# Optimization experiments

Hardware: AMD Instinct MI355X
Metric: run time of the kernel (lower is better)

Reference implementation:

```python
import jax, jax.numpy as jnp
import numpy as np

H = 128          # hidden_channels
L = 2            # num_layers
E = 400000       # edges per relation
N_ATOM = 600000
N = (20000, 20000, 10000)  # node counts: 0=Chemical, 1=Gene, 2=Assay
OUT = 2          # out_channels
# (src_type, dst_type) per relation, matching the HeteroConv_att dict order
RELS = ((0,2),(0,2),(0,1),(0,1),(0,1),(2,1),(1,1),(2,0),(2,0),(1,0),(1,0),(1,0),(1,2))
R = len(RELS)
NEG_SLOPE = 0.2  # GATv2 LeakyReLU slope


def setup_inputs() -> dict:
    key = jax.random.key(0)
    ks = jax.random.split(key, 16)
    sc = 1.0 / np.sqrt(H)
    x_atom  = jax.random.normal(ks[0], (N_ATOM, H), jnp.float32)
    x_chem  = jax.random.normal(ks[1], (N[0], H), jnp.float32)
    x_gene  = jax.random.normal(ks[2], (N[1], H), jnp.float32)
    x_assay = jax.random.normal(ks[3], (N[2], H), jnp.float32)
    hyper_dst = jax.random.randint(ks[4], (N_ATOM,), 0, N[0], jnp.int32)
    ei = []
    for r, (s, d) in enumerate(RELS):
        src = jax.random.randint(jax.random.fold_in(ks[5], 2 * r), (E,), 0, N[s], jnp.int32)
        dst = jax.random.randint(jax.random.fold_in(ks[5], 2 * r + 1), (E,), 0, N[d], jnp.int32)
        ei.append(jnp.stack([src, dst]))
    edge_index_rel = jnp.stack(ei)  # [R, 2, E]
    W_mol = jax.random.normal(ks[6], (H, H), jnp.float32) * sc
    Wl    = jax.random.normal(ks[7], (L, R, H, H), jnp.float32) * sc
    Wr    = jax.random.normal(ks[8], (L, R, H, H), jnp.float32) * sc
    bl    = jnp.zeros((L, R, H), jnp.float32)
    br    = jnp.zeros((L, R, H), jnp.float32)
    att_a = jax.random.normal(ks[9], (L, R, H), jnp.float32) * sc
    cb    = jnp.zeros((L, R, H), jnp.float32)  # GATv2 output bias
    ln_g  = jnp.ones((L, 3, H), jnp.float32)   # LayerNorm gamma per (layer, node type)
    ln_b  = jnp.zeros((L, 3, H), jnp.float32)
    Wp    = jax.random.normal(ks[10], (H, OUT), jnp.float32) * sc
    bp    = jnp.zeros((OUT,), jnp.float32)
    return dict(x_atom=x_atom, x_chem=x_chem, x_gene=x_gene, x_assay=x_assay,
                W_mol=W_mol, Wl=Wl, Wr=Wr, bl=bl, br=br, att_a=att_a, cb=cb,
                ln_g=ln_g, ln_b=ln_b, Wp=Wp, bp=bp,
                hyper_dst=hyper_dst, edge_index_rel=edge_index_rel,
                chemical_label_task=0)


def _gatv2(x_src, x_dst, src, dst, Wl, Wr, bl, br, a, cb, n_dst):
    # GATv2Conv, single head, add_self_loops=False, share_weights=False
    xl = x_src @ Wl + bl                              # [Ns, H]
    xr = x_dst @ Wr + br                              # [Nd, H]
    e = jax.nn.leaky_relu(xl[src] + xr[dst], NEG_SLOPE) @ a  # [E]
    m = jax.ops.segment_max(e, dst, num_segments=n_dst)      # per-dst max
    ex = jnp.exp(e - m[dst])
    denom = jax.ops.segment_sum(ex, dst, num_segments=n_dst)
    alpha = ex / jnp.maximum(denom[dst], 1e-16)
    out = jax.ops.segment_sum(alpha[:, None] * xl[src], dst, num_segments=n_dst)
    return out + cb


def _layernorm(x, g, b):
    mu = x.mean(-1, keepdims=True)
    v = ((x - mu) ** 2).mean(-1, keepdims=True)
    return (x - mu) / jnp.sqrt(v + 1e-5) * g + b


def reference(x_atom, x_chem, x_gene, x_assay, W_mol, Wl, Wr, bl, br, att_a, cb,
              ln_g, ln_b, Wp, bp, hyper_dst, edge_index_rel, chemical_label_task):
    # molecular encoder (modeled as a linear projection over atom features)
    atom_enc = x_atom @ W_mol
    # bottom_up: mean-aggregate Atom -> Chemical, then add dst (Chemical) features
    ones = jnp.ones((N_ATOM,), atom_enc.dtype)
    cnt = jax.ops.segment_sum(ones, hyper_dst, num_segments=N[0])
    mean_agg = jax.ops.segment_sum(atom_enc, hyper_dst, num_segments=N[0]) \
               / jnp.maximum(cnt, 1.0)[:, None]
    xs = [mean_agg + x_chem, x_gene, x_assay]  # Chemical, Gene, Assay
    for l in range(L):
        agg = [jnp.zeros((N[t], H), x_chem.dtype) for t in range(3)]
        for r, (s, d) in enumerate(RELS):
            src = edge_index_rel[r, 0]
            dst = edge_index_rel[r, 1]
            out = _gatv2(xs[s], xs[d], src, dst, Wl[l, r], Wr[l, r], bl[l, r],
                         br[l, r], att_a[l, r], cb[l, r], N[d])
            agg[d] = agg[d] + out  # aggr='sum' across relations per dst type
        xs = [jax.nn.relu(_layernorm(agg[t], ln_g[l, t], ln_b[l, t])) for t in range(3)]
    return xs[0] @ Wp + bp  # pred_layer on Chemical nodes -> [N_chem, OUT]
```

## Files before the change

kernel.cpp:

```cpp
#include <hip/hip_runtime.h>
#include <math.h>

#define H 128
#define NLAYER 2
#define EDG 400000
#define NATOM 600000
#define NREL 13
#define SEGS 14
#define RDX 256
#define TILE 4096
#define NPAIR 5800000

typedef unsigned short u16;
typedef unsigned int u32;
using short8  = __attribute__((ext_vector_type(8))) short;
using ushort8 = __attribute__((ext_vector_type(8))) unsigned short;
using floatx4 = __attribute__((ext_vector_type(4))) float;

static constexpr int NODE_N[3]   = {20000, 20000, 10000};
static constexpr int TYPE_OFF[3] = {0, 20000, 40000};
static constexpr int SRC_T[NREL] = {0,0,0,0,0,2,1,2,2,1,1,1,1};
static constexpr int DST_T[NREL] = {2,2,1,1,1,1,1,0,0,0,0,0,2};

static constexpr int NREL_OF[3]    = {5, 5, 3};
static constexpr int RELS_OF[3][5] = {{7,8,9,10,11},{2,3,4,5,6},{0,1,12}};

static constexpr int XOFF_S[NREL] = {0,20000,40000,60000,80000,100000,110000,130000,140000,150000,170000,190000,210000};
static constexpr int XOFF_D[NREL] = {0,10000,20000,40000,60000,80000,100000,120000,140000,160000,180000,200000,220000};
#define XTOT 230000

static constexpr int SEG_N[SEGS]  = {20000,10000,10000,20000,20000,20000,20000,20000,20000,20000,20000,20000,20000,10000};
static constexpr int SEG_RO[SEGS] = {0,20001,30002,40003,60004,80005,100006,120007,140008,160009,180010,200011,220012,240013};
#define RP_TOTAL 250016

static constexpr int    SLEN[SEGS] = {600000,EDG,EDG,EDG,EDG,EDG,EDG,EDG,EDG,EDG,EDG,EDG,EDG,EDG};
static constexpr size_t SPOFF[SEGS] = {0,600000,1000000,1400000,1800000,2200000,2600000,3000000,3400000,3800000,4200000,4600000,5000000,5400000};
static constexpr int    RNB[SEGS]  = {147,98,98,98,98,98,98,98,98,98,98,98,98,98};
static constexpr int    RBHOFF[SEGS] = {0,37632,62720,87808,112896,137984,163072,188160,213248,238336,263424,288512,313600,338688};
#define BH_TOTAL 363776

__device__ __forceinline__ float wave_reduce_sum(float v) {
#pragma unroll
  for (int off = 32; off > 0; off >>= 1) v += __shfl_xor(v, off, 64);
  return v;
}

__device__ __forceinline__ u16 f2bf(float f) {
  union { float f; u32 u; } c; c.f = f;
  u32 u = c.u + 0x7fffu + ((c.u >> 16) & 1u);
  return (u16)(u >> 16);
}
__device__ __forceinline__ float bf2f(u16 h) { union { u32 i; float f; } c; c.i = (u32)h << 16; return c.f; }
__device__ __forceinline__ float bflo(u32 u) { union { u32 i; float f; } c; c.i = u << 16; return c.f; }
__device__ __forceinline__ float bfhi(u32 u) { union { u32 i; float f; } c; c.i = u & 0xffff0000u; return c.f; }


__global__ __launch_bounds__(256) void radix_init(const int* __restrict__ hyper,
                                                  const int* __restrict__ ei,
                                                  int2* __restrict__ A) {
  int s = blockIdx.y;
  int i = blockIdx.x * 256 + threadIdx.x;
  if (i >= SLEN[s]) return;
  int2 p;
  if (s == 0) { p.x = hyper[i]; p.y = i; }
  else {
    int r = s - 1;
    p.x = ei[(size_t)(r * 2 + 1) * EDG + i];
    p.y = ei[(size_t)(r * 2) * EDG + i];
  }
  A[SPOFF[s] + i] = p;
}

__global__ __launch_bounds__(256) void radix_count(const int2* __restrict__ in,
                                                   int* __restrict__ bh, int shift) {
  int s = blockIdx.y, bx = blockIdx.x;
  int nb = RNB[s];
  if (bx >= nb) return;
  __shared__ int h[RDX];
  int t = threadIdx.x;
  h[t] = 0;
  __syncthreads();
  int len = SLEN[s];
  size_t poff = SPOFF[s];
#pragma unroll
  for (int i = 0; i < 16; ++i) {
    int p = bx * TILE + i * 256 + t;
    if (p < len) atomicAdd(&h[(in[poff + p].x >> shift) & 255], 1);
  }
  __syncthreads();
  bh[RBHOFF[s] + t * nb + bx] = h[t];
}

__global__ __launch_bounds__(256) void radix_scan(int* __restrict__ bh) {
  int s = blockIdx.x;
  int total = RNB[s] * RDX;
  int off = RBHOFF[s];
  __shared__ int sums[256];
  int t = threadIdx.x;
  int chunk = (total + 255) >> 8;
  int b = t * chunk, e = min(b + chunk, total);
  int acc = 0;
  for (int i = b; i < e; ++i) acc += bh[off + i];
  sums[t] = acc;
  __syncthreads();
  for (int o2 = 1; o2 < 256; o2 <<= 1) {
    int v = (t >= o2) ? sums[t - o2] : 0;
    __syncthreads();
    sums[t] += v;
    __syncthreads();
  }
  int pre = t ? sums[t - 1] : 0;
  for (int i = b; i < e; ++i) { int c = bh[off + i]; bh[off + i] = pre; pre += c; }
}

__global__ __launch_bounds__(256) void radix_scatter(const int2* __restrict__ in,
                                                     int2* __restrict__ out,
                                                     const int* __restrict__ bh, int shift) {
  int s = blockIdx.y, bx = blockIdx.x;
  int nb = RNB[s];
  if (bx >= nb) return;
  __shared__ int2 stg[TILE];
  __shared__ int wc[4][RDX];
  __shared__ int pw[4][RDX];
  __shared__ int basev[RDX];
  __shared__ int lstart[RDX];
  __shared__ int delta[RDX];
  int t = threadIdx.x;
  int lane = t & 63, w = t >> 6;
  unsigned long long lmask = (1ull << lane) - 1ull;
  int len = SLEN[s];
  size_t poff = SPOFF[s];
  int2 kv[16]; int dg[16]; int rk[16];
  basev[t] = 0;
#pragma unroll
  for (int i = 0; i < 16; ++i) {
    int p = bx * TILE + i * 256 + t;
    kv[i] = (p < len) ? in[poff + p] : make_int2(0, 0);
  }
  __syncthreads();
  for (int i = 0; i < 16; ++i) {
    int p = bx * TILE + i * 256 + t;
    bool valid = p < len;
    int d = (kv[i].x >> shift) & 255;
    wc[0][t] = 0; wc[1][t] = 0; wc[2][t] = 0; wc[3][t] = 0;
    __syncthreads();
    unsigned long long m = __ballot(valid);
#pragma unroll
    for (int b2 = 0; b2 < 8; ++b2) {
      unsigned long long bal = __ballot((d >> b2) & 1);
      m &= ((d >> b2) & 1) ? bal : ~bal;
    }
    int riw = __popcll(m & lmask);
    if (valid && riw == 0) wc[w][d] = __popcll(m);
    __syncthreads();
    int s0 = 0;
#pragma unroll
    for (int ww = 0; ww < 4; ++ww) { pw[ww][t] = s0; s0 += wc[ww][t]; }
    __syncthreads();
    dg[i] = d;
    rk[i] = basev[d] + pw[w][d] + riw;
    __syncthreads();
    basev[t] += s0;
    __syncthreads();
  }
  int tot = basev[t];
  pw[0][t] = tot;
  __syncthreads();
  for (int o2 = 1; o2 < 256; o2 <<= 1) {
    int v = (t >= o2) ? pw[0][t - o2] : 0;
    __syncthreads();
    pw[0][t] += v;
    __syncthreads();
  }
  int ls = pw[0][t] - tot;
  lstart[t] = ls;
  delta[t] = bh[RBHOFF[s] + t * nb + bx] - ls;
  __syncthreads();
#pragma unroll
  for (int i = 0; i < 16; ++i) {
    int p = bx * TILE + i * 256 + t;
    if (p < len) stg[lstart[dg[i]] + rk[i]] = kv[i];
  }
  __syncthreads();
  int vc = min(len - bx * TILE, TILE);
#pragma unroll
  for (int i = 0; i < 16; ++i) {
    int p = i * 256 + t;
    if (p < vc) {
      int2 pr = stg[p];
      int d = (pr.x >> shift) & 255;
      out[poff + delta[d] + p] = pr;
    }
  }
}

__global__ __launch_bounds__(256) void build_rp(const int2* __restrict__ A, int* __restrict__ rp) {
  int s = blockIdx.y;
  int len = SLEN[s];
  int j = blockIdx.x * 256 + threadIdx.x;
  if (j >= len) return;
  size_t poff = SPOFF[s];
  int ro = SEG_RO[s];
  int k = A[poff + j].x;
  int kprev = (j == 0) ? -1 : A[poff + j - 1].x;
  for (int d = kprev + 1; d <= k; ++d) rp[ro + d] = j;
  if (j == len - 1) {
    int n = SEG_N[s];
    for (int d = k + 1; d <= n; ++d) rp[ro + d] = len;
  }
}


__global__ __launch_bounds__(256) void mean_atoms(const float* __restrict__ x_atom,
                                                  const int* __restrict__ rp,
                                                  const int2* __restrict__ pairs,
                                                  float* __restrict__ Mean) {
  int wave = (blockIdx.x * blockDim.x + threadIdx.x) >> 6;
  int lane = threadIdx.x & 63;
  int g = lane >> 5, l32 = lane & 31;
  int chem = wave * 2 + g;
  if (chem >= 20000) return;
  int b = rp[chem], e = rp[chem + 1];
  float4 s = make_float4(0.f, 0.f, 0.f, 0.f);
  for (int j = b; j < e; ++j) {
    int a = pairs[j].y;
    float4 v = *(const float4*)(x_atom + (size_t)a * H + l32 * 4);
    s.x += v.x; s.y += v.y; s.z += v.z; s.w += v.w;
  }
  float inv = 1.0f / fmaxf((float)(e - b), 1.0f);
  float4 o; o.x = s.x * inv; o.y = s.y * inv; o.z = s.z * inv; o.w = s.w * inv;
  *(float4*)(Mean + (size_t)chem * H + l32 * 4) = o;
}


__global__ __launch_bounds__(256) void proj_kernel(
    const float* __restrict__ X, const float* __restrict__ W,
    const float* __restrict__ Res, float* __restrict__ Y, int N) {
  int r0 = blockIdx.x * 64;
  if (r0 >= N) return;
  __shared__ float Xs[64][132];
  int tid = threadIdx.x;
#pragma unroll
  for (int i = 0; i < 8; ++i) {
    int f = tid + 256 * i;
    int row = f >> 5, c4 = (f & 31) << 2;
    float4 v = make_float4(0.f, 0.f, 0.f, 0.f);
    if (r0 + row < N) v = *(const float4*)(X + (size_t)(r0 + row) * H + c4);
    *(float4*)&Xs[row][c4] = v;
  }
  __syncthreads();
  int trow = tid >> 5, tcol = tid & 31;
  float acc[8][4] = {};
#pragma unroll 4
  for (int k = 0; k < 128; ++k) {
    float4 w = *(const float4*)(W + k * H + tcol * 4);
#pragma unroll
    for (int i = 0; i < 8; ++i) {
      float xv = Xs[trow * 8 + i][k];
      acc[i][0] = fmaf(xv, w.x, acc[i][0]);
      acc[i][1] = fmaf(xv, w.y, acc[i][1]);
      acc[i][2] = fmaf(xv, w.z, acc[i][2]);
      acc[i][3] = fmaf(xv, w.w, acc[i][3]);
    }
  }
#pragma unroll
  for (int i = 0; i < 8; ++i) {
    int row = r0 + trow * 8 + i;
    if (row < N) {
      float4 rv = *(const float4*)(Res + (size_t)row * H + tcol * 4);
      float4 ov;
      ov.x = acc[i][0] + rv.x; ov.y = acc[i][1] + rv.y;
      ov.z = acc[i][2] + rv.z; ov.w = acc[i][3] + rv.w;
      *(float4*)(Y + (size_t)row * H + tcol * 4) = ov;
    }
  }
}


__global__ __launch_bounds__(256) void conv_xs(const float* __restrict__ xs,
                                               const float* __restrict__ x_gene,
                                               const float* __restrict__ x_assay,
                                               u16* __restrict__ xsb) {
  int idx = (blockIdx.x * 256 + threadIdx.x) * 4;
  if (idx >= 50000 * H) return;
  int row = idx >> 7;
  const float* src;
  if (row < 20000)      src = xs + idx;
  else if (row < 40000) src = x_gene + (idx - 20000 * H);
  else                  src = x_assay + (idx - 40000 * H);
  float4 v = *(const float4*)src;
  u32 p0 = (u32)f2bf(v.x) | ((u32)f2bf(v.y) << 16);
  u32 p1 = (u32)f2bf(v.z) | ((u32)f2bf(v.w) << 16);
  u32* o = (u32*)(xsb + idx);
  o[0] = p0; o[1] = p1;
}

__global__ __launch_bounds__(256) void conv_weights(const float* __restrict__ Wl,
                                                    const float* __restrict__ Wr,
                                                    u16* __restrict__ WB) {
  int mat = blockIdx.x;
  int side = blockIdx.y;
  const float* W = (side ? Wr : Wl) + (size_t)mat * H * H;
  u16* O = WB + ((size_t)mat * 2 + side) * H * H;
  for (int f = threadIdx.x; f < H * H; f += 256) {
    int n = f >> 7, k = f & 127;
    O[f] = f2bf(W[k * H + n]);
  }
}


__global__ __launch_bounds__(256) void proj_mfma(
    const u16* __restrict__ xsb, const u16* __restrict__ WB,
    const float* __restrict__ bl, const float* __restrict__ br,
    u16* __restrict__ XLb, u16* __restrict__ XRb, int layer) {
  int by = blockIdx.y;
  int r = by >> 1, side = by & 1;
  int typ = side ? DST_T[r] : SRC_T[r];
  int N = NODE_N[typ];
  int r0 = blockIdx.x * 64;
  if (r0 >= N) return;
  const u16* X = xsb + (size_t)TYPE_OFF[typ] * H;
  const u16* W = WB + ((size_t)(layer * NREL + r) * 2 + side) * H * H;
  const float* bias = (side ? br : bl) + (size_t)(layer * NREL + r) * H;
  u16* Y = side ? (XRb + (size_t)XOFF_D[r] * H) : (XLb + (size_t)XOFF_S[r] * H);

  __shared__ u16 Xs[64 * 136];
  __shared__ u16 Ws[128 * 136];
  int tid = threadIdx.x;
#pragma unroll
  for (int i = 0; i < 4; ++i) {
    int f = tid + 256 * i;
    int row = f >> 4, seg = f & 15;
    ushort8 v = {};
    if (r0 + row < N) v = *(const ushort8*)(X + (size_t)(r0 + row) * H + seg * 8);
    *(ushort8*)(Xs + row * 136 + seg * 8) = v;
  }
#pragma unroll
  for (int i = 0; i < 8; ++i) {
    int f = tid + 256 * i;
    int row = f >> 4, seg = f & 15;
    *(ushort8*)(Ws + row * 136 + seg * 8) = *(const ushort8*)(W + row * H + seg * 8);
  }
  __syncthreads();

  int w = tid >> 6, lane = tid & 63;
  int g = lane >> 4, l16 = lane & 15;
  floatx4 acc[4][2] = {};
#pragma unroll
  for (int kt = 0; kt < 4; ++kt) {
    int k0 = kt * 32 + g * 8;
    short8 a[4], b[2];
#pragma unroll
    for (int rt = 0; rt < 4; ++rt) a[rt] = *(const short8*)(Xs + (rt * 16 + l16) * 136 + k0);
#pragma unroll
    for (int ct = 0; ct < 2; ++ct) b[ct] = *(const short8*)(Ws + (w * 32 + ct * 16 + l16) * 136 + k0);
#pragma unroll
    for (int rt = 0; rt < 4; ++rt)
#pragma unroll
      for (int ct = 0; ct < 2; ++ct)
        acc[rt][ct] = __builtin_amdgcn_mfma_f32_16x16x32_bf16(a[rt], b[ct], acc[rt][ct], 0, 0, 0);
  }
  __syncthreads();
  float bv0 = bias[w * 32 + l16];
  float bv1 = bias[w * 32 + 16 + l16];
#pragma unroll
  for (int rt = 0; rt < 4; ++rt)
#pragma unroll
    for (int ct = 0; ct < 2; ++ct) {
      float bv = ct ? bv1 : bv0;
      int col = w * 32 + ct * 16 + l16;
#pragma unroll
      for (int reg = 0; reg < 4; ++reg) {
        int row = rt * 16 + g * 4 + reg;
        Xs[row * 136 + col] = f2bf(acc[rt][ct][reg] + bv);
      }
    }
  __syncthreads();
#pragma unroll
  for (int i = 0; i < 4; ++i) {
    int f = tid + 256 * i;
    int row = f >> 4, seg = f & 15;
    if (r0 + row < N)
      *(ushort8*)(Y + (size_t)(r0 + row) * H + seg * 8) = *(const ushort8*)(Xs + row * 136 + seg * 8);
  }
}


__global__ __launch_bounds__(256) void gat_fused(
    const u16* __restrict__ XLb, const u16* __restrict__ XRb,
    const int* __restrict__ rp, const int2* __restrict__ A,
    const float* __restrict__ att_a, const float* __restrict__ cbv,
    float* __restrict__ agg, int layer, int dt) {
  int wave = (blockIdx.x * blockDim.x + threadIdx.x) >> 6;
  int lane = threadIdx.x & 63;
  int g = lane >> 4, l16 = lane & 15;
  int d = wave * 4 + g;
  int Nd = NODE_N[dt];
  bool dv = d < Nd;
  int dd = dv ? d : Nd - 1;
  float o[8] = {};
  int nr = NREL_OF[dt];
  for (int rr = 0; rr < nr; ++rr) {
    int r = RELS_OF[dt][rr];
    size_t wi = (size_t)layer * NREL + r;
    const u16* XL = XLb + (size_t)XOFF_S[r] * H;
    const u16* XR = XRb + (size_t)XOFF_D[r] * H;
    ushort8 uxr = *(const ushort8*)(XR + (size_t)dd * H + l16 * 8);
    float xr[8];
#pragma unroll
    for (int c = 0; c < 8; ++c) xr[c] = bf2f((u16)uxr[c]);
    float4 a0 = *(const float4*)(att_a + wi * H + l16 * 8);
    float4 a1 = *(const float4*)(att_a + wi * H + l16 * 8 + 4);
    float av[8] = {a0.x, a0.y, a0.z, a0.w, a1.x, a1.y, a1.z, a1.w};
    const int* rpr = rp + SEG_RO[r + 1];
    const int2* pe = A + SPOFF[r + 1];
    int b = dv ? rpr[dd] : 0;
    int e = dv ? rpr[dd + 1] : 0;
    float m = -1e30f, s = 0.f;
    float V[8] = {};
    for (int j = b; j < e; ++j) {
      int src = pe[j].y;
      ushort8 uxl = *(const ushort8*)(XL + (size_t)src * H + l16 * 8);
      float xl[8];
      float t = 0.f;
#pragma unroll
      for (int c = 0; c < 8; ++c) {
        xl[c] = bf2f((u16)uxl[c]);
        float v = xl[c] + xr[c];
        float lr = v > 0.f ? v : 0.2f * v;
        t = fmaf(av[c], lr, t);
      }
      t += __shfl_xor(t, 1, 64);
      t += __shfl_xor(t, 2, 64);
      t += __shfl_xor(t, 4, 64);
      t += __shfl_xor(t, 8, 64);
      float nm = fmaxf(m, t);
      float sc = __expf(m - nm);
      float wgt = __expf(t - nm);
      s = s * sc + wgt;
#pragma unroll
      for (int c = 0; c < 8; ++c) V[c] = V[c] * sc + wgt * xl[c];
      m = nm;
    }
    if (s > 0.f) {
      float inv = 1.0f / s;
#pragma unroll
      for (int c = 0; c < 8; ++c) o[c] += V[c] * inv;
    }
    float4 c0 = *(const float4*)(cbv + wi * H + l16 * 8);
    float4 c1 = *(const float4*)(cbv + wi * H + l16 * 8 + 4);
    o[0] += c0.x; o[1] += c0.y; o[2] += c0.z; o[3] += c0.w;
    o[4] += c1.x; o[5] += c1.y; o[6] += c1.z; o[7] += c1.w;
  }
  if (dv) {
    float* ap = agg + (size_t)(TYPE_OFF[dt] + d) * H + l16 * 8;
    *(float4*)ap       = make_float4(o[0], o[1], o[2], o[3]);
    *(float4*)(ap + 4) = make_float4(o[4], o[5], o[6], o[7]);
  }
}


__global__ __launch_bounds__(256) void ln_relu_kernel(const float* __restrict__ agg,
                                                      const float* __restrict__ g,
                                                      const float* __restrict__ b,
                                                      u16* __restrict__ xsb) {
  int row = (blockIdx.x * blockDim.x + threadIdx.x) >> 6;
  int lane = threadIdx.x & 63;
  if (row >= 50000) return;
  int t = row < 20000 ? 0 : (row < 40000 ? 1 : 2);
  float2 x = *(const float2*)(agg + (size_t)row * H + 2 * lane);
  float mu = wave_reduce_sum(x.x + x.y) * (1.f / 128.f);
  float d0 = x.x - mu, d1 = x.y - mu;
  float var = wave_reduce_sum(d0 * d0 + d1 * d1) * (1.f / 128.f);
  float inv = 1.0f / sqrtf(var + 1e-5f);
  float2 gg = *(const float2*)(g + t * H + 2 * lane);
  float2 bb = *(const float2*)(b + t * H + 2 * lane);
  float o0 = fmaxf(d0 * inv * gg.x + bb.x, 0.f);
  float o1 = fmaxf(d1 * inv * gg.y + bb.y, 0.f);
  u32 pk = (u32)f2bf(o0) | ((u32)f2bf(o1) << 16);
  *(u32*)(xsb + (size_t)row * H + 2 * lane) = pk;
}


__global__ __launch_bounds__(256) void pred_kernel(const u16* __restrict__ xsb,
                                                   const float* __restrict__ Wp,
                                                   const float* __restrict__ bp,
                                                   float* __restrict__ out) {
  int row = (blockIdx.x * blockDim.x + threadIdx.x) >> 6;
  int lane = threadIdx.x & 63;
  if (row >= 20000) return;
  u32 u = *(const u32*)(xsb + (size_t)row * H + 2 * lane);
  float x0 = bflo(u), x1 = bfhi(u);
  float4 w = *(const float4*)(Wp + 4 * lane);
  float pA = x0 * w.x + x1 * w.z;
  float pB = x0 * w.y + x1 * w.w;
  pA = wave_reduce_sum(pA);
  pB = wave_reduce_sum(pB);
  if (lane == 0) {
    out[(size_t)row * 2 + 0] = pA + bp[0];
    out[(size_t)row * 2 + 1] = pB + bp[1];
  }
}


extern "C" void kernel_launch(void* const* d_in, const int* in_sizes, int n_in,
                              void* d_out, int out_size, void* d_ws, size_t ws_size,
                              hipStream_t stream) {
  (void)in_sizes; (void)n_in; (void)out_size; (void)ws_size;
  const float* x_atom  = (const float*)d_in[0];
  const float* x_chem  = (const float*)d_in[1];
  const float* x_gene  = (const float*)d_in[2];
  const float* x_assay = (const float*)d_in[3];
  const float* W_mol   = (const float*)d_in[4];
  const float* Wl      = (const float*)d_in[5];
  const float* Wr      = (const float*)d_in[6];
  const float* bl      = (const float*)d_in[7];
  const float* br      = (const float*)d_in[8];
  const float* att_a   = (const float*)d_in[9];
  const float* cb      = (const float*)d_in[10];
  const float* ln_g    = (const float*)d_in[11];
  const float* ln_b    = (const float*)d_in[12];
  const float* Wp      = (const float*)d_in[13];
  const float* bp      = (const float*)d_in[14];
  const int*   hyper   = (const int*)d_in[15];
  const int*   ei      = (const int*)d_in[16];
  float* out = (float*)d_out;

  float* ws = (float*)d_ws;
  size_t o = 0;
  float* xs   = ws + o; o += (size_t)50000 * H;
  float* agg  = ws + o; o += (size_t)50000 * H;
  float* Mean = ws + o; o += (size_t)20000 * H;
  int2*  A    = (int2*)(ws + o); o += (size_t)2 * NPAIR;
  int2*  Bp2  = (int2*)(ws + o); o += (size_t)2 * NPAIR;
  int*   rp   = (int*)(ws + o); o += RP_TOTAL;
  int*   bh   = (int*)(ws + o); o += BH_TOTAL;
  u16*   xsb  = (u16*)(ws + o); o += (size_t)50000 * H / 2;
  u16*   WB   = (u16*)(ws + o); o += (size_t)52 * H * H / 2;
  u16*   XLb  = (u16*)(ws + o); o += (size_t)XTOT * H / 2;
  u16*   XRb  = (u16*)(ws + o); o += (size_t)XTOT * H / 2;

  dim3 b256(256);

  radix_init<<<dim3(2344, SEGS), b256, 0, stream>>>(hyper, ei, A);
  radix_count<<<dim3(147, SEGS), b256, 0, stream>>>(A, bh, 0);
  radix_scan<<<SEGS, b256, 0, stream>>>(bh);
  radix_scatter<<<dim3(147, SEGS), b256, 0, stream>>>(A, Bp2, bh, 0);
  radix_count<<<dim3(147, SEGS), b256, 0, stream>>>(Bp2, bh, 8);
  radix_scan<<<SEGS, b256, 0, stream>>>(bh);
  radix_scatter<<<dim3(147, SEGS), b256, 0, stream>>>(Bp2, A, bh, 8);
  build_rp<<<dim3(2344, SEGS), b256, 0, stream>>>(A, rp);

  mean_atoms<<<dim3(20000 / 8), b256, 0, stream>>>(x_atom, rp, A, Mean);
  proj_kernel<<<dim3(313), b256, 0, stream>>>(Mean, W_mol, x_chem, xs, 20000);
  conv_xs<<<dim3(6250), b256, 0, stream>>>(xs, x_gene, x_assay, xsb);
  conv_weights<<<dim3(26, 2), b256, 0, stream>>>(Wl, Wr, WB);

  for (int l = 0; l < NLAYER; ++l) {
    proj_mfma<<<dim3(313, 26), b256, 0, stream>>>(xsb, WB, bl, br, XLb, XRb, l);
    for (int dt = 0; dt < 3; ++dt)
      gat_fused<<<dim3((NODE_N[dt] + 15) / 16), b256, 0, stream>>>(
          XLb, XRb, rp, A, att_a, cb, agg, l, dt);
    ln_relu_kernel<<<dim3(50000 / 4), b256, 0, stream>>>(agg, ln_g + l * 3 * H, ln_b + l * 3 * H, xsb);
  }
  pred_kernel<<<dim3(20000 / 4), b256, 0, stream>>>(xsb, Wp, bp, out);
}
```

Baseline: 1.710 ms.

## Pack edge pairs into 32-bit keys, merge GAT launches, unroll edge loop by two

Edge (dst,src) pairs are packed into a single u32 (dst<<15|src) instead of int2, which halves radix-sort and CSR traffic. The sort uses bits 15 and 23 as digit positions so the two passes key on dst. The three per-type GAT launches are merged into one launch over all 50000 nodes. The GAT inner loop processes two edges per iteration so loads overlap and one online-softmax rescale serves both edges. The chemical projection writes bf16 directly, removing the fp32 xs buffer and part of the conversion pass; the packing relies on src<32768 and dst<131072.

```diff
diff --git a/kernel.cpp b/kernel.cpp
--- a/kernel.cpp
+++ b/kernel.cpp
@@ -9,7 +9,6 @@
 #define SEGS 14
 #define RDX 256
 #define TILE 4096
-#define NPAIR 5800000
 
 typedef unsigned short u16;
 typedef unsigned int u32;
@@ -33,9 +32,8 @@
 static constexpr int SEG_RO[SEGS] = {0,20001,30002,40003,60004,80005,100006,120007,140008,160009,180010,200011,220012,240013};
 #define RP_TOTAL 250016
 
-static constexpr int    SLEN[SEGS] = {600000,EDG,EDG,EDG,EDG,EDG,EDG,EDG,EDG,EDG,EDG,EDG,EDG,EDG};
-static constexpr size_t SPOFF[SEGS] = {0,600000,1000000,1400000,1800000,2200000,2600000,3000000,3400000,3800000,4200000,4600000,5000000,5400000};
-static constexpr int    RNB[SEGS]  = {147,98,98,98,98,98,98,98,98,98,98,98,98,98};
+static constexpr int    SLEN[SEGS]   = {600000,EDG,EDG,EDG,EDG,EDG,EDG,EDG,EDG,EDG,EDG,EDG,EDG,EDG};
+static constexpr int    RNB[SEGS]    = {147,98,98,98,98,98,98,98,98,98,98,98,98,98};
 static constexpr int    RBHOFF[SEGS] = {0,37632,62720,87808,112896,137984,163072,188160,213248,238336,263424,288512,313600,338688};
 #define BH_TOTAL 363776
 
@@ -54,38 +52,40 @@
 __device__ __forceinline__ float bflo(u32 u) { union { u32 i; float f; } c; c.i = u << 16; return c.f; }
 __device__ __forceinline__ float bfhi(u32 u) { union { u32 i; float f; } c; c.i = u & 0xffff0000u; return c.f; }
 
-
-__global__ __launch_bounds__(256) void radix_init(const int* __restrict__ hyper,
-                                                  const int* __restrict__ ei,
-                                                  int2* __restrict__ A) {
-  int s = blockIdx.y;
+__device__ __forceinline__ int digof(u32 v, int shift) { return (int)((v >> shift) & 255u); }
+__device__ __forceinline__ int digof(int2 v, int shift) { return (v.x >> shift) & 255; }
+
+
+__global__ __launch_bounds__(256) void radix_init_a(const int* __restrict__ hyper, int2* __restrict__ Aa) {
   int i = blockIdx.x * 256 + threadIdx.x;
-  if (i >= SLEN[s]) return;
-  int2 p;
-  if (s == 0) { p.x = hyper[i]; p.y = i; }
-  else {
-    int r = s - 1;
-    p.x = ei[(size_t)(r * 2 + 1) * EDG + i];
-    p.y = ei[(size_t)(r * 2) * EDG + i];
-  }
-  A[SPOFF[s] + i] = p;
-}
-
-__global__ __launch_bounds__(256) void radix_count(const int2* __restrict__ in,
-                                                   int* __restrict__ bh, int shift) {
-  int s = blockIdx.y, bx = blockIdx.x;
+  if (i >= NATOM) return;
+  Aa[i] = make_int2(hyper[i], i);
+}
+
+__global__ __launch_bounds__(256) void radix_init_e(const int* __restrict__ ei, u32* __restrict__ Ae) {
+  int r = blockIdx.y;
+  int i = blockIdx.x * 256 + threadIdx.x;
+  if (i >= EDG) return;
+  u32 src = (u32)ei[(size_t)(r * 2) * EDG + i];
+  u32 dst = (u32)ei[(size_t)(r * 2 + 1) * EDG + i];
+  Ae[(size_t)r * EDG + i] = (dst << 15) | src;
+}
+
+template <typename T>
+__global__ __launch_bounds__(256) void radix_count_t(const T* __restrict__ in,
+                                                     int* __restrict__ bh, int shift, int seg0) {
+  int s = seg0 + blockIdx.y, bx = blockIdx.x;
   int nb = RNB[s];
-  if (bx >= nb) return;
   __shared__ int h[RDX];
   int t = threadIdx.x;
   h[t] = 0;
   __syncthreads();
   int len = SLEN[s];
-  size_t poff = SPOFF[s];
+  size_t poff = (s == 0) ? 0 : (size_t)(s - 1) * EDG;
 #pragma unroll
   for (int i = 0; i < 16; ++i) {
     int p = bx * TILE + i * 256 + t;
-    if (p < len) atomicAdd(&h[(in[poff + p].x >> shift) & 255], 1);
+    if (p < len) atomicAdd(&h[digof(in[poff + p], shift)], 1);
   }
   __syncthreads();
   bh[RBHOFF[s] + t * nb + bx] = h[t];
@@ -113,13 +113,13 @@
   for (int i = b; i < e; ++i) { int c = bh[off + i]; bh[off + i] = pre; pre += c; }
 }
 
-__global__ __launch_bounds__(256) void radix_scatter(const int2* __restrict__ in,
-                                                     int2* __restrict__ out,
-                                                     const int* __restrict__ bh, int shift) {
-  int s = blockIdx.y, bx = blockIdx.x;
+template <typename T>
+__global__ __launch_bounds__(256) void radix_scat_t(const T* __restrict__ in,
+                                                    T* __restrict__ out,
+                                                    const int* __restrict__ bh, int shift, int seg0) {
+  int s = seg0 + blockIdx.y, bx = blockIdx.x;
   int nb = RNB[s];
-  if (bx >= nb) return;
-  __shared__ int2 stg[TILE];
+  __shared__ T stg[TILE];
   __shared__ int wc[4][RDX];
   __shared__ int pw[4][RDX];
   __shared__ int basev[RDX];
@@ -129,19 +129,19 @@
   int lane = t & 63, w = t >> 6;
   unsigned long long lmask = (1ull << lane) - 1ull;
   int len = SLEN[s];
-  size_t poff = SPOFF[s];
-  int2 kv[16]; int dg[16]; int rk[16];
+  size_t poff = (s == 0) ? 0 : (size_t)(s - 1) * EDG;
+  T kv[16]; int dg[16]; int rk[16];
   basev[t] = 0;
 #pragma unroll
   for (int i = 0; i < 16; ++i) {
     int p = bx * TILE + i * 256 + t;
-    kv[i] = (p < len) ? in[poff + p] : make_int2(0, 0);
+    kv[i] = (p < len) ? in[poff + p] : T{};
   }
   __syncthreads();
   for (int i = 0; i < 16; ++i) {
     int p = bx * TILE + i * 256 + t;
     bool valid = p < len;
-    int d = (kv[i].x >> shift) & 255;
+    int d = digof(kv[i], shift);
     wc[0][t] = 0; wc[1][t] = 0; wc[2][t] = 0; wc[3][t] = 0;
     __syncthreads();
     unsigned long long m = __ballot(valid);
@@ -187,27 +187,35 @@
   for (int i = 0; i < 16; ++i) {
     int p = i * 256 + t;
     if (p < vc) {
-      int2 pr = stg[p];
-      int d = (pr.x >> shift) & 255;
+      T pr = stg[p];
+      int d = digof(pr, shift);
       out[poff + delta[d] + p] = pr;
     }
   }
 }
 
-__global__ __launch_bounds__(256) void build_rp(const int2* __restrict__ A, int* __restrict__ rp) {
-  int s = blockIdx.y;
-  int len = SLEN[s];
+__global__ __launch_bounds__(256) void build_rp_a(const int2* __restrict__ Aa, int* __restrict__ rp) {
   int j = blockIdx.x * 256 + threadIdx.x;
-  if (j >= len) return;
-  size_t poff = SPOFF[s];
-  int ro = SEG_RO[s];
-  int k = A[poff + j].x;
-  int kprev = (j == 0) ? -1 : A[poff + j - 1].x;
+  if (j >= NATOM) return;
+  int k = Aa[j].x;
+  int kprev = (j == 0) ? -1 : Aa[j - 1].x;
+  for (int d = kprev + 1; d <= k; ++d) rp[d] = j;
+  if (j == NATOM - 1)
+    for (int d = k + 1; d <= 20000; ++d) rp[d] = NATOM;
+}
+
+__global__ __launch_bounds__(256) void build_rp_e(const u32* __restrict__ Ae, int* __restrict__ rp) {
+  int r = blockIdx.y;
+  int j = blockIdx.x * 256 + threadIdx.x;
+  if (j >= EDG) return;
+  const u32* Ar = Ae + (size_t)r * EDG;
+  int ro = SEG_RO[r + 1];
+  int n = SEG_N[r + 1];
+  int k = (int)(Ar[j] >> 15);
+  int kprev = (j == 0) ? -1 : (int)(Ar[j - 1] >> 15);
   for (int d = kprev + 1; d <= k; ++d) rp[ro + d] = j;
-  if (j == len - 1) {
-    int n = SEG_N[s];
-    for (int d = k + 1; d <= n; ++d) rp[ro + d] = len;
-  }
+  if (j == EDG - 1)
+    for (int d = k + 1; d <= n; ++d) rp[ro + d] = EDG;
 }
 
 
@@ -235,7 +243,7 @@
 
 __global__ __launch_bounds__(256) void proj_kernel(
     const float* __restrict__ X, const float* __restrict__ W,
-    const float* __restrict__ Res, float* __restrict__ Y, int N) {
+    const float* __restrict__ Res, u16* __restrict__ Yb, int N) {
   int r0 = blockIdx.x * 64;
   if (r0 >= N) return;
   __shared__ float Xs[64][132];
@@ -268,26 +276,21 @@
     int row = r0 + trow * 8 + i;
     if (row < N) {
       float4 rv = *(const float4*)(Res + (size_t)row * H + tcol * 4);
-      float4 ov;
-      ov.x = acc[i][0] + rv.x; ov.y = acc[i][1] + rv.y;
-      ov.z = acc[i][2] + rv.z; ov.w = acc[i][3] + rv.w;
-      *(float4*)(Y + (size_t)row * H + tcol * 4) = ov;
-    }
-  }
-}
-
-
-__global__ __launch_bounds__(256) void conv_xs(const float* __restrict__ xs,
-                                               const float* __restrict__ x_gene,
+      u32 lo = (u32)f2bf(acc[i][0] + rv.x) | ((u32)f2bf(acc[i][1] + rv.y) << 16);
+      u32 hi = (u32)f2bf(acc[i][2] + rv.z) | ((u32)f2bf(acc[i][3] + rv.w) << 16);
+      *(uint2*)(Yb + (size_t)row * H + tcol * 4) = make_uint2(lo, hi);
+    }
+  }
+}
+
+
+__global__ __launch_bounds__(256) void conv_xs(const float* __restrict__ x_gene,
                                                const float* __restrict__ x_assay,
                                                u16* __restrict__ xsb) {
-  int idx = (blockIdx.x * 256 + threadIdx.x) * 4;
+  int idx = 20000 * H + (blockIdx.x * 256 + threadIdx.x) * 4;
   if (idx >= 50000 * H) return;
   int row = idx >> 7;
-  const float* src;
-  if (row < 20000)      src = xs + idx;
-  else if (row < 40000) src = x_gene + (idx - 20000 * H);
-  else                  src = x_assay + (idx - 40000 * H);
+  const float* src = (row < 40000) ? x_gene + (idx - 20000 * H) : x_assay + (idx - 40000 * H);
   float4 v = *(const float4*)src;
   u32 p0 = (u32)f2bf(v.x) | ((u32)f2bf(v.y) << 16);
   u32 p1 = (u32)f2bf(v.z) | ((u32)f2bf(v.w) << 16);
@@ -388,64 +391,84 @@
 
 __global__ __launch_bounds__(256) void gat_fused(
     const u16* __restrict__ XLb, const u16* __restrict__ XRb,
-    const int* __restrict__ rp, const int2* __restrict__ A,
+    const int* __restrict__ rp, const u32* __restrict__ Ae,
     const float* __restrict__ att_a, const float* __restrict__ cbv,
-    float* __restrict__ agg, int layer, int dt) {
+    float* __restrict__ agg, int layer) {
   int wave = (blockIdx.x * blockDim.x + threadIdx.x) >> 6;
   int lane = threadIdx.x & 63;
   int g = lane >> 4, l16 = lane & 15;
   int d = wave * 4 + g;
-  int Nd = NODE_N[dt];
-  bool dv = d < Nd;
-  int dd = dv ? d : Nd - 1;
+  bool dv = d < 50000;
+  int dd = dv ? d : 49999;
+  int dt = dd < 20000 ? 0 : (dd < 40000 ? 1 : 2);
+  int dl = dd - TYPE_OFF[dt];
   float o[8] = {};
   int nr = NREL_OF[dt];
   for (int rr = 0; rr < nr; ++rr) {
     int r = RELS_OF[dt][rr];
     size_t wi = (size_t)layer * NREL + r;
     const u16* XL = XLb + (size_t)XOFF_S[r] * H;
-    const u16* XR = XRb + (size_t)XOFF_D[r] * H;
-    ushort8 uxr = *(const ushort8*)(XR + (size_t)dd * H + l16 * 8);
-    float xr[8];
-#pragma unroll
-    for (int c = 0; c < 8; ++c) xr[c] = bf2f((u16)uxr[c]);
+    ushort8 uxr = *(const ushort8*)(XRb + (size_t)(XOFF_D[r] + dl) * H + l16 * 8);
     float4 a0 = *(const float4*)(att_a + wi * H + l16 * 8);
     float4 a1 = *(const float4*)(att_a + wi * H + l16 * 8 + 4);
     float av[8] = {a0.x, a0.y, a0.z, a0.w, a1.x, a1.y, a1.z, a1.w};
+    float xr[8];
+#pragma unroll
+    for (int c = 0; c < 8; ++c) xr[c] = bf2f((u16)uxr[c]);
     const int* rpr = rp + SEG_RO[r + 1];
-    const int2* pe = A + SPOFF[r + 1];
-    int b = dv ? rpr[dd] : 0;
-    int e = dv ? rpr[dd + 1] : 0;
+    const u32* pe = Ae + (size_t)r * EDG;
+    int b = dv ? rpr[dl] : 0;
+    int e = dv ? rpr[dl + 1] : 0;
     float m = -1e30f, s = 0.f;
     float V[8] = {};
-    for (int j = b; j < e; ++j) {
-      int src = pe[j].y;
-      ushort8 uxl = *(const ushort8*)(XL + (size_t)src * H + l16 * 8);
-      float xl[8];
+    int j = b;
+    if ((e - b) & 1) {
+      int src = (int)(pe[j] & 32767u);
+      ushort8 u0 = *(const ushort8*)(XL + (size_t)src * H + l16 * 8);
       float t = 0.f;
 #pragma unroll
       for (int c = 0; c < 8; ++c) {
-        xl[c] = bf2f((u16)uxl[c]);
-        float v = xl[c] + xr[c];
-        float lr = v > 0.f ? v : 0.2f * v;
-        t = fmaf(av[c], lr, t);
+        V[c] = bf2f((u16)u0[c]);
+        float v = V[c] + xr[c];
+        t = fmaf(av[c], fmaxf(v, 0.2f * v), t);
       }
-      t += __shfl_xor(t, 1, 64);
-      t += __shfl_xor(t, 2, 64);
-      t += __shfl_xor(t, 4, 64);
-      t += __shfl_xor(t, 8, 64);
-      float nm = fmaxf(m, t);
+      t += __shfl_xor(t, 1, 64); t += __shfl_xor(t, 2, 64);
+      t += __shfl_xor(t, 4, 64); t += __shfl_xor(t, 8, 64);
+      s = 1.0f;
+      m = t;
+      ++j;
+    }
+    for (; j < e; j += 2) {
+      u32 p0 = pe[j], p1 = pe[j + 1];
+      int s0 = (int)(p0 & 32767u), s1 = (int)(p1 & 32767u);
+      ushort8 u0 = *(const ushort8*)(XL + (size_t)s0 * H + l16 * 8);
+      ushort8 u1 = *(const ushort8*)(XL + (size_t)s1 * H + l16 * 8);
+      float xl0[8], xl1[8], t0 = 0.f, t1 = 0.f;
+#pragma unroll
+      for (int c = 0; c < 8; ++c) {
+        xl0[c] = bf2f((u16)u0[c]);
+        xl1[c] = bf2f((u16)u1[c]);
+        float v0 = xl0[c] + xr[c], v1 = xl1[c] + xr[c];
+        t0 = fmaf(av[c], fmaxf(v0, 0.2f * v0), t0);
+        t1 = fmaf(av[c], fmaxf(v1, 0.2f * v1), t1);
+      }
+      t0 += __shfl_xor(t0, 1, 64); t1 += __shfl_xor(t1, 1, 64);
+      t0 += __shfl_xor(t0, 2, 64); t1 += __shfl_xor(t1, 2, 64);
+      t0 += __shfl_xor(t0, 4, 64); t1 += __shfl_xor(t1, 4, 64);
+      t0 += __shfl_xor(t0, 8, 64); t1 += __shfl_xor(t1, 8, 64);
+      float nm = fmaxf(m, fmaxf(t0, t1));
       float sc = __expf(m - nm);
-      float wgt = __expf(t - nm);
-      s = s * sc + wgt;
-#pragma unroll
-      for (int c = 0; c < 8; ++c) V[c] = V[c] * sc + wgt * xl[c];
+      float w0 = __expf(t0 - nm), w1 = __expf(t1 - nm);
+      s = fmaf(s, sc, w0 + w1);
+#pragma unroll
+      for (int c = 0; c < 8; ++c)
+        V[c] = fmaf(V[c], sc, fmaf(w0, xl0[c], w1 * xl1[c]));
       m = nm;
     }
     if (s > 0.f) {
       float inv = 1.0f / s;
 #pragma unroll
-      for (int c = 0; c < 8; ++c) o[c] += V[c] * inv;
+      for (int c = 0; c < 8; ++c) o[c] = fmaf(V[c], inv, o[c]);
     }
     float4 c0 = *(const float4*)(cbv + wi * H + l16 * 8);
     float4 c1 = *(const float4*)(cbv + wi * H + l16 * 8 + 4);
@@ -453,7 +476,7 @@
     o[4] += c1.x; o[5] += c1.y; o[6] += c1.z; o[7] += c1.w;
   }
   if (dv) {
-    float* ap = agg + (size_t)(TYPE_OFF[dt] + d) * H + l16 * 8;
+    float* ap = agg + (size_t)dd * H + l16 * 8;
     *(float4*)ap       = make_float4(o[0], o[1], o[2], o[3]);
     *(float4*)(ap + 4) = make_float4(o[4], o[5], o[6], o[7]);
   }
@@ -528,11 +551,12 @@
 
   float* ws = (float*)d_ws;
   size_t o = 0;
-  float* xs   = ws + o; o += (size_t)50000 * H;
   float* agg  = ws + o; o += (size_t)50000 * H;
   float* Mean = ws + o; o += (size_t)20000 * H;
-  int2*  A    = (int2*)(ws + o); o += (size_t)2 * NPAIR;
-  int2*  Bp2  = (int2*)(ws + o); o += (size_t)2 * NPAIR;
+  int2*  Aa   = (int2*)(ws + o); o += (size_t)2 * NATOM;
+  int2*  Ba   = (int2*)(ws + o); o += (size_t)2 * NATOM;
+  u32*   Ae   = (u32*)(ws + o); o += (size_t)NREL * EDG;
+  u32*   Be   = (u32*)(ws + o); o += (size_t)NREL * EDG;
   int*   rp   = (int*)(ws + o); o += RP_TOTAL;
   int*   bh   = (int*)(ws + o); o += BH_TOTAL;
   u16*   xsb  = (u16*)(ws + o); o += (size_t)50000 * H / 2;
@@ -542,25 +566,29 @@
 
   dim3 b256(256);
 
-  radix_init<<<dim3(2344, SEGS), b256, 0, stream>>>(hyper, ei, A);
-  radix_count<<<dim3(147, SEGS), b256, 0, stream>>>(A, bh, 0);
+  radix_init_a<<<dim3(2344), b256, 0, stream>>>(hyper, Aa);
+  radix_init_e<<<dim3(1563, 13), b256, 0, stream>>>(ei, Ae);
+  radix_count_t<int2><<<dim3(147, 1), b256, 0, stream>>>(Aa, bh, 0, 0);
+  radix_count_t<u32><<<dim3(98, 13), b256, 0, stream>>>(Ae, bh, 15, 1);
   radix_scan<<<SEGS, b256, 0, stream>>>(bh);
-  radix_scatter<<<dim3(147, SEGS), b256, 0, stream>>>(A, Bp2, bh, 0);
-  radix_count<<<dim3(147, SEGS), b256, 0, stream>>>(Bp2, bh, 8);
+  radix_scat_t<int2><<<dim3(147, 1), b256, 0, stream>>>(Aa, Ba, bh, 0, 0);
+  radix_scat_t<u32><<<dim3(98, 13), b256, 0, stream>>>(Ae, Be, bh, 15, 1);
+  radix_count_t<int2><<<dim3(147, 1), b256, 0, stream>>>(Ba, bh, 8, 0);
+  radix_count_t<u32><<<dim3(98, 13), b256, 0, stream>>>(Be, bh, 23, 1);
   radix_scan<<<SEGS, b256, 0, stream>>>(bh);
-  radix_scatter<<<dim3(147, SEGS), b256, 0, stream>>>(Bp2, A, bh, 8);
-  build_rp<<<dim3(2344, SEGS), b256, 0, stream>>>(A, rp);
-
-  mean_atoms<<<dim3(20000 / 8), b256, 0, stream>>>(x_atom, rp, A, Mean);
-  proj_kernel<<<dim3(313), b256, 0, stream>>>(Mean, W_mol, x_chem, xs, 20000);
-  conv_xs<<<dim3(6250), b256, 0, stream>>>(xs, x_gene, x_assay, xsb);
+  radix_scat_t<int2><<<dim3(147, 1), b256, 0, stream>>>(Ba, Aa, bh, 8, 0);
+  radix_scat_t<u32><<<dim3(98, 13), b256, 0, stream>>>(Be, Ae, bh, 23, 1);
+  build_rp_a<<<dim3(2344), b256, 0, stream>>>(Aa, rp);
+  build_rp_e<<<dim3(1563, 13), b256, 0, stream>>>(Ae, rp);
+
+  mean_atoms<<<dim3(20000 / 8), b256, 0, stream>>>(x_atom, rp, Aa, Mean);
+  proj_kernel<<<dim3(313), b256, 0, stream>>>(Mean, W_mol, x_chem, xsb, 20000);
+  conv_xs<<<dim3(3750), b256, 0, stream>>>(x_gene, x_assay, xsb);
   conv_weights<<<dim3(26, 2), b256, 0, stream>>>(Wl, Wr, WB);
 
   for (int l = 0; l < NLAYER; ++l) {
     proj_mfma<<<dim3(313, 26), b256, 0, stream>>>(xsb, WB, bl, br, XLb, XRb, l);
-    for (int dt = 0; dt < 3; ++dt)
-      gat_fused<<<dim3((NODE_N[dt] + 15) / 16), b256, 0, stream>>>(
-          XLb, XRb, rp, A, att_a, cb, agg, l, dt);
+    gat_fused<<<dim3(3125), b256, 0, stream>>>(XLb, XRb, rp, Ae, att_a, cb, agg, l);
     ln_relu_kernel<<<dim3(50000 / 4), b256, 0, stream>>>(agg, ln_g + l * 3 * H, ln_b + l * 3 * H, xsb);
   }
   pred_kernel<<<dim3(20000 / 4), b256, 0, stream>>>(xsb, Wp, bp, out);
```

After: 1.477 ms. 13.6% less time.
